# Optimization experiments

Hardware: AMD Instinct MI355X
Metric: run time of the kernel (lower is better)

The kernel has to match this reference:

```python
import jax, jax.numpy as jnp
import numpy as np

B, S, D, H = 8, 1024, 768, 12
HS = D // H  # 64


def setup_inputs() -> dict:
    key = jax.random.key(0)
    k1, k2, k3 = jax.random.split(key, 3)
    x = jax.random.normal(k1, (B, S, D), dtype=jnp.float32)
    W_attn = jax.random.normal(k2, (D, 3 * H * HS), dtype=jnp.float32) * 0.02
    b_attn = jnp.zeros((3 * H * HS,), dtype=jnp.float32)
    W_proj = jax.random.normal(k3, (H * HS, D), dtype=jnp.float32) * 0.02
    b_proj = jnp.zeros((D,), dtype=jnp.float32)
    return {"x": x, "W_attn": W_attn, "b_attn": b_attn, "W_proj": W_proj, "b_proj": b_proj}


def reference(x, W_attn, b_attn, W_proj, b_proj):
    b, s, d = x.shape
    # qkv projection: [B,S,3*H*HS] -> [B,S,3,H,HS]
    qkv = (x @ W_attn + b_attn).reshape(b, s, 3, H, HS)
    q, k, v = qkv[:, :, 0], qkv[:, :, 1], qkv[:, :, 2]  # each [B,S,H,HS]
    scale = jnp.sqrt(jnp.asarray(HS, dtype=x.dtype))
    # scores: [B,H,Q,K]
    scores = jnp.einsum("bqhd,bkhd->bhqk", q, k) / scale
    causal = jnp.tril(jnp.ones((s, s), dtype=bool))  # [Q,K]
    scores = jnp.where(causal, scores, -jnp.inf)
    attn = jax.nn.softmax(scores, axis=-1)
    # dropout p=0.0 / inference -> identity
    out = jnp.einsum("bhqk,bkhd->bqhd", attn, v).reshape(b, s, H * HS)
    return out @ W_proj + b_proj
```

## Files before the change

kernel.cpp:

```cpp
#include <hip/hip_runtime.h>
#include <hip/hip_bf16.h>
#include <cstdint>
#include <cmath>

constexpr int B  = 8;
constexpr int S  = 1024;
constexpr int D  = 768;
constexpr int H  = 12;
constexpr int HS = 64;
constexpr int QKVN = 3 * D;

typedef __bf16 bf16x8 __attribute__((ext_vector_type(8)));
typedef float  f32x4  __attribute__((ext_vector_type(4)));

#define MFMA16(a, b, c) __builtin_amdgcn_mfma_f32_16x16x32_bf16((a), (b), (c), 0, 0, 0)

__device__ __forceinline__ void gl_lds16(const void* g, void* l) {
  __builtin_amdgcn_global_load_lds(
      (__attribute__((address_space(1))) void*)g,
      (__attribute__((address_space(3))) void*)l,
      16, 0, 0);
}

__device__ __forceinline__ int xcd_swizzle(int bid, int nwg) {
  int chunk = nwg >> 3;
  return (bid & 7) * chunk + (bid >> 3);
}

__global__ __launch_bounds__(256) void convert_f32_bf16(const float* __restrict__ in,
                                                        __bf16* __restrict__ out, int n) {
  int i = (blockIdx.x * 256 + threadIdx.x) * 8;
  if (i >= n) return;
  float4 f0 = *(const float4*)(in + i);
  float4 f1 = *(const float4*)(in + i + 4);
  bf16x8 o;
  o[0] = (__bf16)f0.x; o[1] = (__bf16)f0.y; o[2] = (__bf16)f0.z; o[3] = (__bf16)f0.w;
  o[4] = (__bf16)f1.x; o[5] = (__bf16)f1.y; o[6] = (__bf16)f1.z; o[7] = (__bf16)f1.w;
  *(bf16x8*)(out + i) = o;
}

__global__ __launch_bounds__(256) void transpose_w(const float* __restrict__ W,
                                                   __bf16* __restrict__ Wt,
                                                   int K, int N) {
  __shared__ float tile[64][65];
  const int n0 = blockIdx.x * 64, k0 = blockIdx.y * 64;
  const int t = threadIdx.x;
#pragma unroll
  for (int i = 0; i < 16; ++i) {
    int e = i * 256 + t;
    int r = e >> 6, c = e & 63;
    tile[r][c] = W[(size_t)(k0 + r) * N + n0 + c];
  }
  __syncthreads();
#pragma unroll
  for (int i = 0; i < 16; ++i) {
    int e = i * 256 + t;
    int r = e >> 6, c = e & 63;
    Wt[(size_t)(n0 + r) * K + k0 + c] = (__bf16)tile[c][r];
  }
}

__global__ __launch_bounds__(256) void build_vt(const __bf16* __restrict__ qkv,
                                                __bf16* __restrict__ Vt) {
  __shared__ __bf16 tile[64][65];
  const int s0 = blockIdx.x * 64;
  const int bh = blockIdx.y;
  const int b = bh / H, h = bh % H;
  const int t = threadIdx.x;
#pragma unroll
  for (int i = 0; i < 16; ++i) {
    int e = i * 256 + t;
    int r = e >> 6, c = e & 63;
    tile[r][c] = qkv[(size_t)(b * S + s0 + r) * QKVN + 2 * D + h * HS + c];
  }
  __syncthreads();
#pragma unroll
  for (int i = 0; i < 16; ++i) {
    int e = i * 256 + t;
    int r = e >> 6, c = e & 63;
    Vt[((size_t)(b * H + h) * HS + r) * S + s0 + c] = tile[c][r];
  }
}

template <typename CT>
__global__ __launch_bounds__(256) void gemm_bt(const __bf16* __restrict__ A,
                                               const __bf16* __restrict__ Bt,
                                               const float* __restrict__ bias,
                                               CT* __restrict__ C,
                                               int M, int N, int K) {
  __shared__ __bf16 As[2][128 * 32];
  __shared__ __bf16 Bs[2][128 * 32];
  const int t = threadIdx.x;
  const int w = t >> 6, l = t & 63, lr = l & 15, lg = l >> 4;
  const int wr = w >> 1, wc = w & 1;

  const int nwg = gridDim.x * gridDim.y;
  const int wg = xcd_swizzle(blockIdx.y * gridDim.x + blockIdx.x, nwg);
  const int m0 = (wg / gridDim.x) * 128, n0 = (wg % gridDim.x) * 128;

  f32x4 acc[4][4] = {};

  auto stage = [&](int buf, int k0) {
#pragma unroll
    for (int i = 0; i < 2; ++i) {
      int e = i * 256 + t;
      int row = e >> 2;
      int cb = (e & 3) * 16;
      gl_lds16((const char*)(A + (size_t)(m0 + row) * K + k0) + cb, (char*)&As[buf][0] + e * 16);
      gl_lds16((const char*)(Bt + (size_t)(n0 + row) * K + k0) + cb, (char*)&Bs[buf][0] + e * 16);
    }
  };

  stage(0, 0);
  asm volatile("s_waitcnt vmcnt(0)" ::: "memory");
  __syncthreads();

  const int nk = K / 32;
  int cur = 0;
  for (int kt = 0; kt < nk; ++kt) {
    if (kt + 1 < nk) stage(cur ^ 1, (kt + 1) * 32);

    bf16x8 a[4], bb[4];
#pragma unroll
    for (int mt = 0; mt < 4; ++mt)
      a[mt] = *(const bf16x8*)&As[cur][(wr * 64 + mt * 16 + lr) * 32 + lg * 8];
#pragma unroll
    for (int nt = 0; nt < 4; ++nt)
      bb[nt] = *(const bf16x8*)&Bs[cur][(wc * 64 + nt * 16 + lr) * 32 + lg * 8];
#pragma unroll
    for (int mt = 0; mt < 4; ++mt)
#pragma unroll
      for (int nt = 0; nt < 4; ++nt)
        acc[mt][nt] = MFMA16(a[mt], bb[nt], acc[mt][nt]);

    asm volatile("s_waitcnt vmcnt(0)" ::: "memory");
    __syncthreads();
    cur ^= 1;
  }

#pragma unroll
  for (int mt = 0; mt < 4; ++mt)
#pragma unroll
    for (int nt = 0; nt < 4; ++nt) {
#pragma unroll
      for (int r = 0; r < 4; ++r) {
        int row = m0 + wr * 64 + mt * 16 + lg * 4 + r;
        int col = n0 + wc * 64 + nt * 16 + lr;
        float v = acc[mt][nt][r] + bias[col];
        C[(size_t)row * N + col] = (CT)v;
      }
    }
}

__global__ __launch_bounds__(256, 3) void attn_kernel(const __bf16* __restrict__ qkv,
                                                      const __bf16* __restrict__ Vt,
                                                      __bf16* __restrict__ ao) {
  __shared__ __bf16 KV[2][2][64 * 64];
  __shared__ __bf16 Pb[2][4][16 * 64];

  const int t = threadIdx.x;
  const int w = t >> 6, l = t & 63, lr = l & 15, lg = l >> 4;

  const int wg = xcd_swizzle(blockIdx.y * gridDim.x + blockIdx.x, 768);
  const int qb = wg & 7;
  const int bh = wg >> 3;
  const int qA = qb, qB = 15 - qb;
  const int b = bh / H, h = bh % H;
  const size_t qbase = (size_t)(b * S) * QKVN;

  const __bf16* Kg = qkv + qbase + D + h * HS;
  const __bf16* Vg = Vt + (size_t)(b * H + h) * HS * S;

  bf16x8 aqA[2], aqB[2];
  {
    const __bf16* qpA = qkv + qbase + (size_t)(qA * 64 + w * 16 + lr) * QKVN + h * HS + lg * 8;
    aqA[0] = *(const bf16x8*)qpA;
    aqA[1] = *(const bf16x8*)(qpA + 32);
    const __bf16* qpB = qkv + qbase + (size_t)(qB * 64 + w * 16 + lr) * QKVN + h * HS + lg * 8;
    aqB[0] = *(const bf16x8*)qpB;
    aqB[1] = *(const bf16x8*)(qpB + 32);
  }

  f32x4 oA[4] = {}, oB[4] = {};
  f32x4 lsA = {}, lsB = {};
  bf16x8 ones;
#pragma unroll
  for (int j = 0; j < 8; ++j) ones[j] = (__bf16)1.0f;

  const int xr = (lr & 7) << 3;
  const int nit = qB + 1;

  auto stage = [&](int buf, int it) {
    const int kv0 = it * 64;
#pragma unroll
    for (int i = 0; i < 2; ++i) {
      int e = i * 256 + t;
      int row = e >> 3;
      int cb = ((e & 7) * 16) ^ ((row & 7) << 4);
      gl_lds16((const char*)(Kg + (size_t)(kv0 + row) * QKVN) + cb,
               (char*)&KV[buf][0][0] + e * 16);
      gl_lds16((const char*)(Vg + (size_t)row * S + kv0) + cb,
               (char*)&KV[buf][1][0] + e * 16);
    }
  };

  stage(0, 0);
  asm volatile("s_waitcnt vmcnt(0)" ::: "memory");
  __syncthreads();

  const float SCL = 0.18033688011112042f;

  int cur = 0;
  for (int it = 0; it < nit; ++it) {
    if (it + 1 < nit) stage(cur ^ 1, it + 1);

    const __bf16* Ks = &KV[cur][0][0];
    const __bf16* Vs = &KV[cur][1][0];
    const bool doA = (it <= qA);

    f32x4 sA[4] = {}, sB[4] = {};
    __builtin_amdgcn_s_setprio(1);
#pragma unroll
    for (int kk = 0; kk < 2; ++kk) {
      bf16x8 bk[4];
#pragma unroll
      for (int tc = 0; tc < 4; ++tc)
        bk[tc] = *(const bf16x8*)&Ks[(tc * 16 + lr) * 64 + ((kk * 32 + lg * 8) ^ xr)];
#pragma unroll
      for (int tc = 0; tc < 4; ++tc) sB[tc] = MFMA16(aqB[kk], bk[tc], sB[tc]);
      if (doA) {
#pragma unroll
        for (int tc = 0; tc < 4; ++tc) sA[tc] = MFMA16(aqA[kk], bk[tc], sA[tc]);
      }
    }
    __builtin_amdgcn_s_setprio(0);

    __bf16* pwB = &Pb[1][w][0];
    {
      const bool dg = (it == qB);
#pragma unroll
      for (int tc = 0; tc < 4; ++tc)
#pragma unroll
        for (int r = 0; r < 4; ++r) {
          float v = sB[tc][r] * SCL;
          if (dg && (tc * 16 + lr) > (w * 16 + lg * 4 + r)) v = -INFINITY;
          float p = exp2f(v);
          int qrow = lg * 4 + r;
          pwB[qrow * 64 + ((tc * 16 + lr) ^ ((qrow & 7) << 3))] = (__bf16)p;
        }
    }
    __bf16* pwA = &Pb[0][w][0];
    if (doA) {
      const bool dg = (it == qA);
#pragma unroll
      for (int tc = 0; tc < 4; ++tc)
#pragma unroll
        for (int r = 0; r < 4; ++r) {
          float v = sA[tc][r] * SCL;
          if (dg && (tc * 16 + lr) > (w * 16 + lg * 4 + r)) v = -INFINITY;
          float p = exp2f(v);
          int qrow = lg * 4 + r;
          pwA[qrow * 64 + ((tc * 16 + lr) ^ ((qrow & 7) << 3))] = (__bf16)p;
        }
    }

    __builtin_amdgcn_s_setprio(1);
#pragma unroll
    for (int kk = 0; kk < 2; ++kk) {
      bf16x8 apB = *(const bf16x8*)&pwB[lr * 64 + ((kk * 32 + lg * 8) ^ xr)];
      lsB = MFMA16(apB, ones, lsB);
      bf16x8 apA;
      if (doA) {
        apA = *(const bf16x8*)&pwA[lr * 64 + ((kk * 32 + lg * 8) ^ xr)];
        lsA = MFMA16(apA, ones, lsA);
      }
#pragma unroll
      for (int td = 0; td < 4; ++td) {
        bf16x8 bv = *(const bf16x8*)&Vs[(td * 16 + lr) * 64 + ((kk * 32 + lg * 8) ^ xr)];
        oB[td] = MFMA16(apB, bv, oB[td]);
        if (doA) oA[td] = MFMA16(apA, bv, oA[td]);
      }
    }
    __builtin_amdgcn_s_setprio(0);

    asm volatile("s_waitcnt vmcnt(0)" ::: "memory");
    __syncthreads();
    cur ^= 1;
  }

#pragma unroll
  for (int r = 0; r < 4; ++r) {
    const float invA = 1.f / lsA[r];
    const float invB = 1.f / lsB[r];
    const int rowA = qA * 64 + w * 16 + lg * 4 + r;
    const int rowB = qB * 64 + w * 16 + lg * 4 + r;
#pragma unroll
    for (int td = 0; td < 4; ++td) {
      int col = h * HS + td * 16 + lr;
      ao[(size_t)(b * S + rowA) * D + col] = (__bf16)(oA[td][r] * invA);
      ao[(size_t)(b * S + rowB) * D + col] = (__bf16)(oB[td][r] * invB);
    }
  }
}

extern "C" void kernel_launch(void* const* d_in, const int* in_sizes, int n_in,
                              void* d_out, int out_size, void* d_ws, size_t ws_size,
                              hipStream_t stream) {
  const float* x      = (const float*)d_in[0];
  const float* W_attn = (const float*)d_in[1];
  const float* b_attn = (const float*)d_in[2];
  const float* W_proj = (const float*)d_in[3];
  const float* b_proj = (const float*)d_in[4];
  float* out = (float*)d_out;

  char* ws = (char*)d_ws;
  __bf16* xb  = (__bf16*)(ws + 0);
  __bf16* Wat = (__bf16*)(ws + 12582912);
  __bf16* Wpt = (__bf16*)(ws + 16121856);
  __bf16* qkv = (__bf16*)(ws + 17301504);
  __bf16* Vt  = (__bf16*)(ws + 55050240);
  __bf16* ao  = (__bf16*)(ws + 67633152);

  const int nX = B * S * D;

  convert_f32_bf16<<<nX / 8 / 256, 256, 0, stream>>>(x, xb, nX);
  transpose_w<<<dim3(QKVN / 64, D / 64), 256, 0, stream>>>(W_attn, Wat, D, QKVN);
  transpose_w<<<dim3(D / 64, D / 64), 256, 0, stream>>>(W_proj, Wpt, D, D);

  gemm_bt<__bf16><<<dim3(QKVN / 128, (B * S) / 128), 256, 0, stream>>>(
      xb, Wat, b_attn, qkv, B * S, QKVN, D);

  build_vt<<<dim3(S / 64, B * H), 256, 0, stream>>>(qkv, Vt);

  attn_kernel<<<dim3(8, B * H), 256, 0, stream>>>(qkv, Vt, ao);

  gemm_bt<float><<<dim3(D / 128, (B * S) / 128), 256, 0, stream>>>(
      ao, Wpt, b_proj, out, B * S, D, D);
}
```

Measured before the change: 197.1 us.

## Triple-buffer GEMM LDS staging with XOR swizzle and MFMA priority

Moves the bf16 GEMM from a double-buffered to a triple-buffered LDS pipeline. Loads are issued two k-tiles ahead and each iteration waits with a partial vmcnt and a single barrier instead of a full drain plus syncthreads. It also XOR-swizzles the 16-byte LDS chunks by row to cut bank conflicts on the fragment reads, and raises wave priority around the MFMA block. The trade-off is more LDS per block, which may lower occupancy, and the vmcnt(4) count must match the number of outstanding loads per stage.

After: 194.9 us. No clear change (-1.1%).

```diff
diff --git a/kernel.cpp b/kernel.cpp
--- a/kernel.cpp
+++ b/kernel.cpp
@@ -88,8 +88,8 @@
                                                const float* __restrict__ bias,
                                                CT* __restrict__ C,
                                                int M, int N, int K) {
-  __shared__ __bf16 As[2][128 * 32];
-  __shared__ __bf16 Bs[2][128 * 32];
+  __shared__ __bf16 As[3][128 * 32];
+  __shared__ __bf16 Bs[3][128 * 32];
   const int t = threadIdx.x;
   const int w = t >> 6, l = t & 63, lr = l & 15, lg = l >> 4;
   const int wr = w >> 1, wc = w & 1;
@@ -100,43 +100,54 @@
 
   f32x4 acc[4][4] = {};
 
-  auto stage = [&](int buf, int k0) {
+  auto stage = [&](int buf, int kt) {
+    const int k0 = kt * 32;
 #pragma unroll
     for (int i = 0; i < 2; ++i) {
       int e = i * 256 + t;
       int row = e >> 2;
-      int cb = (e & 3) * 16;
+      int c = e & 3;
+      int cb = (c ^ ((row >> 1) & 3)) * 16;
       gl_lds16((const char*)(A + (size_t)(m0 + row) * K + k0) + cb, (char*)&As[buf][0] + e * 16);
       gl_lds16((const char*)(Bt + (size_t)(n0 + row) * K + k0) + cb, (char*)&Bs[buf][0] + e * 16);
     }
   };
 
-  stage(0, 0);
-  asm volatile("s_waitcnt vmcnt(0)" ::: "memory");
-  __syncthreads();
-
-  const int nk = K / 32;
-  int cur = 0;
-  for (int kt = 0; kt < nk; ++kt) {
-    if (kt + 1 < nk) stage(cur ^ 1, (kt + 1) * 32);
-
+  auto compute = [&](int buf) {
     bf16x8 a[4], bb[4];
 #pragma unroll
-    for (int mt = 0; mt < 4; ++mt)
-      a[mt] = *(const bf16x8*)&As[cur][(wr * 64 + mt * 16 + lr) * 32 + lg * 8];
-#pragma unroll
-    for (int nt = 0; nt < 4; ++nt)
-      bb[nt] = *(const bf16x8*)&Bs[cur][(wc * 64 + nt * 16 + lr) * 32 + lg * 8];
+    for (int mt = 0; mt < 4; ++mt) {
+      int row = wr * 64 + mt * 16 + lr;
+      a[mt] = *(const bf16x8*)&As[buf][row * 32 + ((lg ^ ((row >> 1) & 3)) * 8)];
+    }
+#pragma unroll
+    for (int nt = 0; nt < 4; ++nt) {
+      int row = wc * 64 + nt * 16 + lr;
+      bb[nt] = *(const bf16x8*)&Bs[buf][row * 32 + ((lg ^ ((row >> 1) & 3)) * 8)];
+    }
+    __builtin_amdgcn_s_setprio(1);
 #pragma unroll
     for (int mt = 0; mt < 4; ++mt)
 #pragma unroll
       for (int nt = 0; nt < 4; ++nt)
         acc[mt][nt] = MFMA16(a[mt], bb[nt], acc[mt][nt]);
-
-    asm volatile("s_waitcnt vmcnt(0)" ::: "memory");
-    __syncthreads();
-    cur ^= 1;
-  }
+    __builtin_amdgcn_s_setprio(0);
+  };
+
+  const int nk = K / 32;
+  stage(0, 0);
+  stage(1, 1);
+
+  int kt = 0;
+  for (; kt < nk - 1; ++kt) {
+    asm volatile("s_waitcnt vmcnt(4)" ::: "memory");
+    __builtin_amdgcn_s_barrier();
+    if (kt + 2 < nk) stage((kt + 2) % 3, kt + 2);
+    compute(kt % 3);
+  }
+  asm volatile("s_waitcnt vmcnt(0)" ::: "memory");
+  __builtin_amdgcn_s_barrier();
+  compute(kt % 3);
 
 #pragma unroll
   for (int mt = 0; mt < 4; ++mt)
```
